# Performance work log

Hardware: AMD Instinct MI355X
Metric: run time of the kernel (lower is better)

Reference implementation:

```python
import jax, jax.numpy as jnp
import numpy as np

N_NODES = 100000
N_EDGES = 1600000
IN_FEATS = 256
DIMS = [IN_FEATS, 128, 64, 16, 40]


def setup_inputs() -> dict:
    key = jax.random.key(0)
    ks = jax.random.split(key, 3 + 2 * 4)
    x = jax.random.normal(ks[0], (N_NODES, IN_FEATS), dtype=jnp.float32)
    src = jax.random.randint(ks[1], (N_EDGES,), 0, N_NODES)
    dst = jax.random.randint(ks[2], (N_EDGES,), 0, N_NODES)
    inp = {"x": x, "src": src, "dst": dst}
    for i in range(4):
        fan_in = DIMS[i]
        inp[f"W{i+1}"] = jax.random.normal(ks[3 + 2 * i], (DIMS[i], DIMS[i + 1]), dtype=jnp.float32) / np.sqrt(fan_in)
        inp[f"b{i+1}"] = jnp.zeros((DIMS[i + 1],), dtype=jnp.float32)
    return inp


def reference(x, src, dst, W1, b1, W2, b2, W3, b3, W4, b4):
    n = x.shape[0]
    ones = jnp.ones(src.shape[0], dtype=x.dtype)
    # symmetric GCN normalization (DGL norm='both'); clamp deg>=1 like DGL
    deg_out = jnp.maximum(jax.ops.segment_sum(ones, src, num_segments=n), 1.0)
    deg_in = jnp.maximum(jax.ops.segment_sum(ones, dst, num_segments=n), 1.0)
    norm_src = jax.lax.rsqrt(deg_out)[:, None]  # [N,1]
    norm_dst = jax.lax.rsqrt(deg_in)[:, None]   # [N,1]

    def gconv(h, W, b, act):
        # project first (in_feats >= out_feats for every layer, matching DGL ordering)
        h = (h * norm_src) @ W                                   # [N, d_out]
        h = jax.ops.segment_sum(h[src], dst, num_segments=n)      # SpMM aggregate
        h = h * norm_dst + b
        return jax.nn.relu(h) if act else h

    h = gconv(x, W1, b1, True)
    h = gconv(h, W2, b2, True)
    h = gconv(h, W3, b3, True)
    h = gconv(h, W4, b4, False)
    return h
```

## Files before the change

kernel.cpp:

```cpp
#include <hip/hip_runtime.h>


typedef unsigned short ushort_t;
#define CAP 64

__device__ __forceinline__ void gload_lds16(const float4* g, float4* l) {
    __builtin_amdgcn_global_load_lds(
        (const __attribute__((address_space(1))) void*)g,
        (__attribute__((address_space(3))) void*)l, 16, 0, 0);
}

__device__ __forceinline__ ushort_t f2bf(float f) {
    unsigned u = __float_as_uint(f);
    u += 0x7FFFu + ((u >> 16) & 1u);
    return (ushort_t)(u >> 16);
}
__device__ __forceinline__ unsigned pack2bf(float a, float b) {
    return (unsigned)f2bf(a) | ((unsigned)f2bf(b) << 16);
}
__device__ __forceinline__ float nrm_of(int d) {
    return rsqrtf((float)(d > 1 ? d : 1));
}
#define BFLO(u) __uint_as_float((u) << 16)
#define BFHI(u) __uint_as_float((u) & 0xffff0000u)

template<int DIN, int DOUT, int RB, int KT, typename EPI>
__device__ __forceinline__ void proj_body(
        const float* __restrict__ in, const float* __restrict__ W,
        int N, int n0, float4* __restrict__ wlds, float4* __restrict__ xlds,
        EPI&& epi) {
    constexpr int CG  = DOUT / 4;
    constexpr int RPP = 256 / CG;
    constexpr int R4  = RB / RPP;
    constexpr int K4T = KT / 4;
    constexpr int NKT = DIN / KT;
    constexpr int XTILE = RB * K4T;
    constexpr int WTILE = KT * CG;

    const int tid  = threadIdx.x;
    const int wave = tid >> 6;
    const int lane = tid & 63;
    const int rp   = tid / CG;
    const int cg   = tid - rp * CG;

    float4 acc[R4];
#pragma unroll
    for (int r = 0; r < R4; ++r) acc[r] = make_float4(0.f, 0.f, 0.f, 0.f);

    for (int kt = 0; kt < NKT; ++kt) {
        const float4* wsrc = (const float4*)(W + (size_t)kt * KT * DOUT);
#pragma unroll
        for (int j = 0; j < WTILE / 256; ++j) {
            int base = j * 256 + wave * 64;
            gload_lds16(wsrc + base + lane, &wlds[base]);
        }
#pragma unroll
        for (int j = 0; j < XTILE / 256; ++j) {
            int base = j * 256 + wave * 64;
            int fi   = base + lane;
            int row  = fi / K4T;
            int k4   = fi - row * K4T;
            int k4s  = k4 ^ (row & (K4T - 1));
            int grow = n0 + row; if (grow >= N) grow = N - 1;
            const float4* gsrc = (const float4*)(in + (size_t)grow * DIN) + kt * K4T + k4s;
            gload_lds16(gsrc, &xlds[base]);
        }
        __syncthreads();
#pragma unroll 2
        for (int k4 = 0; k4 < K4T; ++k4) {
            float4 w0 = wlds[(k4 * 4 + 0) * CG + cg];
            float4 w1 = wlds[(k4 * 4 + 1) * CG + cg];
            float4 w2 = wlds[(k4 * 4 + 2) * CG + cg];
            float4 w3 = wlds[(k4 * 4 + 3) * CG + cg];
#pragma unroll
            for (int r = 0; r < R4; ++r) {
                int row = rp + r * RPP;
                float4 xv = xlds[row * K4T + (k4 ^ (row & (K4T - 1)))];
                acc[r].x = fmaf(xv.x, w0.x, acc[r].x);
                acc[r].y = fmaf(xv.x, w0.y, acc[r].y);
                acc[r].z = fmaf(xv.x, w0.z, acc[r].z);
                acc[r].w = fmaf(xv.x, w0.w, acc[r].w);
                acc[r].x = fmaf(xv.y, w1.x, acc[r].x);
                acc[r].y = fmaf(xv.y, w1.y, acc[r].y);
                acc[r].z = fmaf(xv.y, w1.z, acc[r].z);
                acc[r].w = fmaf(xv.y, w1.w, acc[r].w);
                acc[r].x = fmaf(xv.z, w2.x, acc[r].x);
                acc[r].y = fmaf(xv.z, w2.y, acc[r].y);
                acc[r].z = fmaf(xv.z, w2.z, acc[r].z);
                acc[r].w = fmaf(xv.z, w2.w, acc[r].w);
                acc[r].x = fmaf(xv.w, w3.x, acc[r].x);
                acc[r].y = fmaf(xv.w, w3.y, acc[r].y);
                acc[r].z = fmaf(xv.w, w3.z, acc[r].z);
                acc[r].w = fmaf(xv.w, w3.w, acc[r].w);
            }
        }
        __syncthreads();
    }
    epi(acc, rp, cg);
}

__device__ __forceinline__ void gather_l1_body(
        int n, int cb, const int* __restrict__ colp, const int* __restrict__ degO,
        const int* __restrict__ degI, const ushort_t* __restrict__ projbf,
        const float* __restrict__ bias, ushort_t* __restrict__ outbf) {
    constexpr int DOUT = 128;
    const int* cl = colp + (size_t)n * CAP;
    int dgi = degI[n];
    int dg = dgi > CAP ? CAP : dgi;
    float acc[8];
#pragma unroll
    for (int k = 0; k < 8; ++k) acc[k] = 0.f;
    int i = 0;
    for (; i + 4 <= dg; i += 4) {
        int4 ss = *(const int4*)(cl + i);
        uint4 v0 = *(const uint4*)(projbf + (size_t)ss.x * DOUT + cb * 8);
        uint4 v1 = *(const uint4*)(projbf + (size_t)ss.y * DOUT + cb * 8);
        uint4 v2 = *(const uint4*)(projbf + (size_t)ss.z * DOUT + cb * 8);
        uint4 v3 = *(const uint4*)(projbf + (size_t)ss.w * DOUT + cb * 8);
        float n0 = nrm_of(degO[ss.x]), n1 = nrm_of(degO[ss.y]);
        float n2 = nrm_of(degO[ss.z]), n3 = nrm_of(degO[ss.w]);
        acc[0] = fmaf(n0, BFLO(v0.x), fmaf(n1, BFLO(v1.x), fmaf(n2, BFLO(v2.x), fmaf(n3, BFLO(v3.x), acc[0]))));
        acc[1] = fmaf(n0, BFHI(v0.x), fmaf(n1, BFHI(v1.x), fmaf(n2, BFHI(v2.x), fmaf(n3, BFHI(v3.x), acc[1]))));
        acc[2] = fmaf(n0, BFLO(v0.y), fmaf(n1, BFLO(v1.y), fmaf(n2, BFLO(v2.y), fmaf(n3, BFLO(v3.y), acc[2]))));
        acc[3] = fmaf(n0, BFHI(v0.y), fmaf(n1, BFHI(v1.y), fmaf(n2, BFHI(v2.y), fmaf(n3, BFHI(v3.y), acc[3]))));
        acc[4] = fmaf(n0, BFLO(v0.z), fmaf(n1, BFLO(v1.z), fmaf(n2, BFLO(v2.z), fmaf(n3, BFLO(v3.z), acc[4]))));
        acc[5] = fmaf(n0, BFHI(v0.z), fmaf(n1, BFHI(v1.z), fmaf(n2, BFHI(v2.z), fmaf(n3, BFHI(v3.z), acc[5]))));
        acc[6] = fmaf(n0, BFLO(v0.w), fmaf(n1, BFLO(v1.w), fmaf(n2, BFLO(v2.w), fmaf(n3, BFLO(v3.w), acc[6]))));
        acc[7] = fmaf(n0, BFHI(v0.w), fmaf(n1, BFHI(v1.w), fmaf(n2, BFHI(v2.w), fmaf(n3, BFHI(v3.w), acc[7]))));
    }
    for (; i < dg; ++i) {
        int s0 = cl[i];
        uint4 v0 = *(const uint4*)(projbf + (size_t)s0 * DOUT + cb * 8);
        float ns0 = nrm_of(degO[s0]);
        acc[0] = fmaf(ns0, BFLO(v0.x), acc[0]);
        acc[1] = fmaf(ns0, BFHI(v0.x), acc[1]);
        acc[2] = fmaf(ns0, BFLO(v0.y), acc[2]);
        acc[3] = fmaf(ns0, BFHI(v0.y), acc[3]);
        acc[4] = fmaf(ns0, BFLO(v0.z), acc[4]);
        acc[5] = fmaf(ns0, BFHI(v0.z), acc[5]);
        acc[6] = fmaf(ns0, BFLO(v0.w), acc[6]);
        acc[7] = fmaf(ns0, BFHI(v0.w), acc[7]);
    }
    float nm = nrm_of(dgi);
    const float* bp = bias + cb * 8;
    float o[8];
#pragma unroll
    for (int k = 0; k < 8; ++k) o[k] = fmaxf(fmaf(acc[k], nm, bp[k]), 0.f);
    uint4 s;
    s.x = pack2bf(o[0], o[1]); s.y = pack2bf(o[2], o[3]);
    s.z = pack2bf(o[4], o[5]); s.w = pack2bf(o[6], o[7]);
    *(uint4*)(outbf + (size_t)n * DOUT + cb * 8) = s;
}

template<int DIN, int DOUT, int RB, int KT>
__global__ void __launch_bounds__(256) k_combA(
        const float* __restrict__ x, const float* __restrict__ W,
        ushort_t* __restrict__ outbf, int N,
        const int* __restrict__ src, const int* __restrict__ dst,
        int* __restrict__ degO, int* __restrict__ degI,
        int* __restrict__ colp, int E, int PB, int HTH, int NSPLIT) {
    constexpr int CG  = DOUT / 4;
    constexpr int RPP = 256 / CG;
    constexpr int R4  = RB / RPP;
    constexpr int K4T = KT / 4;
    __shared__ float4 wlds[KT * CG];
    __shared__ float4 xlds[RB * K4T];

    int bid = blockIdx.x, g = bid / 5, r = bid - g * 5;
    if (r == 4) {
        int i = g * 256 + (int)threadIdx.x;
        for (; i < E; i += HTH) {
            int s = src[i];
            int d = dst[i];
            atomicAdd(&degO[s], 1);
            if (d < NSPLIT) {
                int rk = atomicAdd(&degI[d], 1);
                if (rk < CAP) colp[(size_t)d * CAP + rk] = s;
            }
        }
        return;
    }
    int pidx = g * 4 + r;
    if (pidx >= PB) return;
    int n0 = pidx * RB;
    proj_body<DIN, DOUT, RB, KT>(x, W, N, n0, wlds, xlds,
        [&](float4 (&acc)[R4], int rp, int cg) {
#pragma unroll
            for (int rr = 0; rr < R4; ++rr) {
                int n = n0 + rp + rr * RPP;
                if (n < N) {
                    ushort4 s;
                    s.x = f2bf(acc[rr].x); s.y = f2bf(acc[rr].y);
                    s.z = f2bf(acc[rr].z); s.w = f2bf(acc[rr].w);
                    *(ushort4*)(outbf + (size_t)n * DOUT + cg * 4) = s;
                }
            }
        });
}

__global__ void __launch_bounds__(256) k_combB(
        const int* __restrict__ src, const int* __restrict__ dst,
        int* __restrict__ degI, int* __restrict__ colp,
        const int* __restrict__ degO, const ushort_t* __restrict__ projbf,
        const float* __restrict__ b1, ushort_t* __restrict__ h1bf,
        int NSPLIT, int E, int HTH) {
    int bid = blockIdx.x, g = bid / 5, r = bid - g * 5;
    if (r == 4) {
        int i = g * 256 + (int)threadIdx.x;
        for (; i < E; i += HTH) {
            int d = dst[i];
            if (d >= NSPLIT) {
                int rk = atomicAdd(&degI[d], 1);
                if (rk < CAP) colp[(size_t)d * CAP + rk] = src[i];
            }
        }
        return;
    }
    long t = ((long)(g * 4 + r)) * 256 + threadIdx.x;
    if (t >= (long)NSPLIT * 16) return;
    int n  = (int)(t >> 4);
    int cb = (int)(t & 15);
    gather_l1_body(n, cb, colp, degO, degI, projbf, b1, h1bf);
}

__global__ void __launch_bounds__(256) k_gather_l1(
        const int* __restrict__ colp, const int* __restrict__ degO,
        const int* __restrict__ degI, const ushort_t* __restrict__ projbf,
        const float* __restrict__ bias, ushort_t* __restrict__ outbf,
        int NSPLIT, int N) {
    long t = blockIdx.x * 256L + threadIdx.x;
    if (t >= (long)(N - NSPLIT) * 16) return;
    int n  = NSPLIT + (int)(t >> 4);
    int cb = (int)(t & 15);
    gather_l1_body(n, cb, colp, degO, degI, projbf, bias, outbf);
}

__global__ void __launch_bounds__(256) k_proj_l2bf(
        const ushort_t* __restrict__ in, const int* __restrict__ degO,
        const float* __restrict__ W, ushort_t* __restrict__ outbf, int N) {
    __shared__ float4 wlds[32 * 16];
    __shared__ uint4  xlds[64 * 4];
    const int tid = threadIdx.x;
    const int rp = tid >> 4, cg = tid & 15;
    int n0 = blockIdx.x * 64;

    float4 acc[4];
#pragma unroll
    for (int r = 0; r < 4; ++r) acc[r] = make_float4(0.f, 0.f, 0.f, 0.f);

    for (int kt = 0; kt < 4; ++kt) {
        const float4* wsrc = (const float4*)(W + (size_t)kt * 32 * 64);
        gload_lds16(wsrc + tid, &wlds[tid]);
        gload_lds16(wsrc + 256 + tid, &wlds[256 + tid]);
        {
            int row = tid >> 2, c = tid & 3;
            int cs = c ^ (row & 3);
            int grow = n0 + row; if (grow >= N) grow = N - 1;
            const uint4* gsrc = (const uint4*)(in + (size_t)grow * 128) + kt * 4 + cs;
            gload_lds16((const float4*)gsrc, (float4*)&xlds[tid]);
        }
        __syncthreads();
#pragma unroll
        for (int k8 = 0; k8 < 4; ++k8) {
            float4 w[8];
#pragma unroll
            for (int j = 0; j < 8; ++j) w[j] = wlds[(k8 * 8 + j) * 16 + cg];
#pragma unroll
            for (int r = 0; r < 4; ++r) {
                int row = rp + r * 16;
                uint4 xv = xlds[row * 4 + (k8 ^ (row & 3))];
                float xf[8] = { BFLO(xv.x), BFHI(xv.x), BFLO(xv.y), BFHI(xv.y),
                                BFLO(xv.z), BFHI(xv.z), BFLO(xv.w), BFHI(xv.w) };
#pragma unroll
                for (int j = 0; j < 8; ++j) {
                    acc[r].x = fmaf(xf[j], w[j].x, acc[r].x);
                    acc[r].y = fmaf(xf[j], w[j].y, acc[r].y);
                    acc[r].z = fmaf(xf[j], w[j].z, acc[r].z);
                    acc[r].w = fmaf(xf[j], w[j].w, acc[r].w);
                }
            }
        }
        __syncthreads();
    }
#pragma unroll
    for (int r = 0; r < 4; ++r) {
        int n = n0 + rp + r * 16;
        if (n < N) {
            float nm = nrm_of(degO[n]);
            ushort4 s;
            s.x = f2bf(acc[r].x * nm); s.y = f2bf(acc[r].y * nm);
            s.z = f2bf(acc[r].z * nm); s.w = f2bf(acc[r].w * nm);
            *(ushort4*)(outbf + (size_t)n * 64 + cg * 4) = s;
        }
    }
}

__global__ void __launch_bounds__(256) k_gather_fuse2(
        const int* __restrict__ colp, const int* __restrict__ degO,
        const int* __restrict__ degI, const ushort_t* __restrict__ p2bf,
        const float* __restrict__ b2, const float* __restrict__ W3,
        float* __restrict__ P3, int N) {
    constexpr int DOUT = 64;
    __shared__ float w3s[64 * 16];
    ((float4*)w3s)[threadIdx.x] = ((const float4*)W3)[threadIdx.x];
    __syncthreads();

    long t = blockIdx.x * 256L + threadIdx.x;
    int n = (int)(t >> 3);
    bool valid = n < N;
    if (!valid) n = N - 1;
    int cb = (int)(t & 7);
    int lane = threadIdx.x & 63;
    int gb = lane & ~7;

    const int* cl = colp + (size_t)n * CAP;
    int dgi = degI[n];
    int dg = dgi > CAP ? CAP : dgi;
    float acc[8];
#pragma unroll
    for (int k = 0; k < 8; ++k) acc[k] = 0.f;
    int i = 0;
    for (; i + 4 <= dg; i += 4) {
        int4 ss = *(const int4*)(cl + i);
        uint4 v0 = *(const uint4*)(p2bf + (size_t)ss.x * DOUT + cb * 8);
        uint4 v1 = *(const uint4*)(p2bf + (size_t)ss.y * DOUT + cb * 8);
        uint4 v2 = *(const uint4*)(p2bf + (size_t)ss.z * DOUT + cb * 8);
        uint4 v3 = *(const uint4*)(p2bf + (size_t)ss.w * DOUT + cb * 8);
        acc[0] += BFLO(v0.x) + BFLO(v1.x) + BFLO(v2.x) + BFLO(v3.x);
        acc[1] += BFHI(v0.x) + BFHI(v1.x) + BFHI(v2.x) + BFHI(v3.x);
        acc[2] += BFLO(v0.y) + BFLO(v1.y) + BFLO(v2.y) + BFLO(v3.y);
        acc[3] += BFHI(v0.y) + BFHI(v1.y) + BFHI(v2.y) + BFHI(v3.y);
        acc[4] += BFLO(v0.z) + BFLO(v1.z) + BFLO(v2.z) + BFLO(v3.z);
        acc[5] += BFHI(v0.z) + BFHI(v1.z) + BFHI(v2.z) + BFHI(v3.z);
        acc[6] += BFLO(v0.w) + BFLO(v1.w) + BFLO(v2.w) + BFLO(v3.w);
        acc[7] += BFHI(v0.w) + BFHI(v1.w) + BFHI(v2.w) + BFHI(v3.w);
    }
    for (; i < dg; ++i) {
        int s0 = cl[i];
        uint4 v0 = *(const uint4*)(p2bf + (size_t)s0 * DOUT + cb * 8);
        acc[0] += BFLO(v0.x); acc[1] += BFHI(v0.x);
        acc[2] += BFLO(v0.y); acc[3] += BFHI(v0.y);
        acc[4] += BFLO(v0.z); acc[5] += BFHI(v0.z);
        acc[6] += BFLO(v0.w); acc[7] += BFHI(v0.w);
    }
    float nm = nrm_of(dgi);
    float ns = nrm_of(degO[n]);
    const float* bp = b2 + cb * 8;
    float o[8];
#pragma unroll
    for (int k = 0; k < 8; ++k)
        o[k] = fmaxf(fmaf(acc[k], nm, bp[k]), 0.f) * ns;
    float y0 = 0.f, y1 = 0.f;
#pragma unroll
    for (int k = 0; k < 64; ++k) {
        float v = __shfl(o[k & 7], gb + (k >> 3), 64);
        y0 = fmaf(v, w3s[k * 16 + 2 * cb], y0);
        y1 = fmaf(v, w3s[k * 16 + 2 * cb + 1], y1);
    }
    if (valid) *(float2*)(P3 + (size_t)n * 16 + 2 * cb) = make_float2(y0, y1);
}

__global__ void __launch_bounds__(256) k_gather_l3(
        const int* __restrict__ colp, const int* __restrict__ degO,
        const int* __restrict__ degI, const float* __restrict__ proj,
        const float* __restrict__ bias, float* __restrict__ out, int N) {
    long t = blockIdx.x * 256L + threadIdx.x;
    if (t >= (long)N * 4) return;
    int n  = (int)(t >> 2);
    int cg = (int)(t & 3);
    const int* cl = colp + (size_t)n * CAP;
    int dgi = degI[n];
    int dg = dgi > CAP ? CAP : dgi;
    float4 a0 = make_float4(0.f, 0.f, 0.f, 0.f);
    float4 a1 = make_float4(0.f, 0.f, 0.f, 0.f);
    float4 a2 = make_float4(0.f, 0.f, 0.f, 0.f);
    float4 a3 = make_float4(0.f, 0.f, 0.f, 0.f);
    int i = 0;
    for (; i + 4 <= dg; i += 4) {
        int4 ss = *(const int4*)(cl + i);
        float4 v0 = *(const float4*)(proj + (size_t)ss.x * 16 + cg * 4);
        float4 v1 = *(const float4*)(proj + (size_t)ss.y * 16 + cg * 4);
        float4 v2 = *(const float4*)(proj + (size_t)ss.z * 16 + cg * 4);
        float4 v3 = *(const float4*)(proj + (size_t)ss.w * 16 + cg * 4);
        a0.x += v0.x; a0.y += v0.y; a0.z += v0.z; a0.w += v0.w;
        a1.x += v1.x; a1.y += v1.y; a1.z += v1.z; a1.w += v1.w;
        a2.x += v2.x; a2.y += v2.y; a2.z += v2.z; a2.w += v2.w;
        a3.x += v3.x; a3.y += v3.y; a3.z += v3.z; a3.w += v3.w;
    }
    for (; i < dg; ++i) {
        int s0 = cl[i];
        float4 v0 = *(const float4*)(proj + (size_t)s0 * 16 + cg * 4);
        a0.x += v0.x; a0.y += v0.y; a0.z += v0.z; a0.w += v0.w;
    }
    float4 s = make_float4(a0.x + a1.x + a2.x + a3.x, a0.y + a1.y + a2.y + a3.y,
                           a0.z + a1.z + a2.z + a3.z, a0.w + a1.w + a2.w + a3.w);
    float nm = nrm_of(dgi);
    float ns = nrm_of(degO[n]);
    float4 b = *(const float4*)(bias + cg * 4);
    float4 o;
    o.x = fmaxf(fmaf(s.x, nm, b.x), 0.f) * ns;
    o.y = fmaxf(fmaf(s.y, nm, b.y), 0.f) * ns;
    o.z = fmaxf(fmaf(s.z, nm, b.z), 0.f) * ns;
    o.w = fmaxf(fmaf(s.w, nm, b.w), 0.f) * ns;
    *(float4*)(out + (size_t)n * 16 + cg * 4) = o;
}

__global__ void __launch_bounds__(256) k_gather_fuse4(
        const int* __restrict__ colp, const int* __restrict__ degI,
        const float* __restrict__ t4, const float* __restrict__ W4,
        const float* __restrict__ b4, float* __restrict__ out, int N) {
    __shared__ float w4s[16 * 40];
    __shared__ float b4s[40];
    for (int i = threadIdx.x; i < 160; i += 256)
        ((float4*)w4s)[i] = ((const float4*)W4)[i];
    if (threadIdx.x < 40) b4s[threadIdx.x] = b4[threadIdx.x];
    __syncthreads();

    long t = blockIdx.x * 256L + threadIdx.x;
    int n = (int)(t >> 2);
    bool valid = n < N;
    if (!valid) n = N - 1;
    int cg = (int)(t & 3);
    int lane = threadIdx.x & 63;
    int gb = lane & ~3;

    const int* cl = colp + (size_t)n * CAP;
    int dgi = degI[n];
    int dg = dgi > CAP ? CAP : dgi;
    float4 a0 = make_float4(0.f, 0.f, 0.f, 0.f);
    float4 a1 = make_float4(0.f, 0.f, 0.f, 0.f);
    int i = 0;
    for (; i + 2 <= dg; i += 2) {
        int2 ss = *(const int2*)(cl + i);
        float4 v0 = *(const float4*)(t4 + (size_t)ss.x * 16 + cg * 4);
        float4 v1 = *(const float4*)(t4 + (size_t)ss.y * 16 + cg * 4);
        a0.x += v0.x; a0.y += v0.y; a0.z += v0.z; a0.w += v0.w;
        a1.x += v1.x; a1.y += v1.y; a1.z += v1.z; a1.w += v1.w;
    }
    if (i < dg) {
        int s0 = cl[i];
        float4 v0 = *(const float4*)(t4 + (size_t)s0 * 16 + cg * 4);
        a0.x += v0.x; a0.y += v0.y; a0.z += v0.z; a0.w += v0.w;
    }
    float av[4] = { a0.x + a1.x, a0.y + a1.y, a0.z + a1.z, a0.w + a1.w };

    float y[10];
#pragma unroll
    for (int jj = 0; jj < 10; ++jj) y[jj] = 0.f;
#pragma unroll
    for (int k = 0; k < 16; ++k) {
        float v = __shfl(av[k & 3], gb + (k >> 2), 64);
        const float* wr = w4s + k * 40 + cg * 10;
#pragma unroll
        for (int jj = 0; jj < 10; ++jj) y[jj] = fmaf(v, wr[jj], y[jj]);
    }
    if (valid) {
        float nm = nrm_of(dgi);
        float* dp = out + (size_t)n * 40 + cg * 10;
        const float* bp = b4s + cg * 10;
#pragma unroll
        for (int jj = 0; jj < 10; ++jj) dp[jj] = fmaf(y[jj], nm, bp[jj]);
    }
}

static inline int cdiv(long a, int b) { return (int)((a + b - 1) / b); }

extern "C" void kernel_launch(void* const* d_in, const int* in_sizes, int n_in,
                              void* d_out, int out_size, void* d_ws, size_t ws_size,
                              hipStream_t stream) {
    const float* x   = (const float*)d_in[0];
    const int*   src = (const int*)d_in[1];
    const int*   dst = (const int*)d_in[2];
    const float* W1 = (const float*)d_in[3];  const float* b1 = (const float*)d_in[4];
    const float* W2 = (const float*)d_in[5];  const float* b2 = (const float*)d_in[6];
    const float* W3 = (const float*)d_in[7];  const float* b3 = (const float*)d_in[8];
    const float* W4 = (const float*)d_in[9];  const float* b4 = (const float*)d_in[10];

    const int N = in_sizes[0] / 256;
    const int E = in_sizes[1];
    const int NSPLIT = ((N / 2) + 63) / 64 * 64;

    int* ws_i = (int*)d_ws;
    int* degO   = ws_i;
    int* degI   = ws_i + N;
    int* colp   = ws_i + 2 * (size_t)N;
    float* projb = (float*)(ws_i + 2 * (size_t)N + (size_t)N * CAP);
    float* hbuf  = projb + (size_t)N * 64;
    ushort_t* projbf = (ushort_t*)projb;
    ushort_t* h1bf   = (ushort_t*)hbuf;
    float* P3 = projb + (size_t)N * 32;

    int PB  = cdiv(N, 64);
    int G5A = cdiv(PB, 4);
    int HTHA = G5A * 256;

    long tA = (long)NSPLIT * 16;
    int GBB = cdiv(tA, 256);
    int G5B = cdiv(GBB, 4);
    int HTHB = G5B * 256;

    hipMemsetAsync(degO, 0, 2 * (size_t)N * sizeof(int), stream);
    k_combA<256, 128, 64, 32><<<5 * G5A, 256, 0, stream>>>(
        x, W1, projbf, N, src, dst, degO, degI, colp, E, PB, HTHA, NSPLIT);

    k_combB<<<5 * G5B, 256, 0, stream>>>(
        src, dst, degI, colp, degO, projbf, b1, h1bf, NSPLIT, E, HTHB);

    k_gather_l1<<<cdiv((long)(N - NSPLIT) * 16, 256), 256, 0, stream>>>(
        colp, degO, degI, projbf, b1, h1bf, NSPLIT, N);

    k_proj_l2bf<<<cdiv(N, 64), 256, 0, stream>>>(h1bf, degO, W2, projbf, N);
    k_gather_fuse2<<<cdiv((long)N * 8, 256), 256, 0, stream>>>(
        colp, degO, degI, projbf, b2, W3, P3, N);

    k_gather_l3<<<cdiv((long)N * 4, 256), 256, 0, stream>>>(
        colp, degO, degI, P3, b3, hbuf, N);

    k_gather_fuse4<<<cdiv((long)N * 4, 256), 256, 0, stream>>>(
        colp, degI, hbuf, W4, b4, (float*)d_out, N);
}
```

Baseline: 343.4 us.

## Split CSR build and layer-1 gather into three node ranges for deeper overlap

```diff
diff --git a/kernel.cpp b/kernel.cpp
--- a/kernel.cpp
+++ b/kernel.cpp
@@ -158,7 +158,7 @@
         ushort_t* __restrict__ outbf, int N,
         const int* __restrict__ src, const int* __restrict__ dst,
         int* __restrict__ degO, int* __restrict__ degI,
-        int* __restrict__ colp, int E, int PB, int HTH, int NSPLIT) {
+        int* __restrict__ colp, int E, int PB, int HTH, int S1) {
     constexpr int CG  = DOUT / 4;
     constexpr int RPP = 256 / CG;
     constexpr int R4  = RB / RPP;
@@ -173,7 +173,7 @@
             int s = src[i];
             int d = dst[i];
             atomicAdd(&degO[s], 1);
-            if (d < NSPLIT) {
+            if (d < S1) {
                 int rk = atomicAdd(&degI[d], 1);
                 if (rk < CAP) colp[(size_t)d * CAP + rk] = s;
             }
@@ -198,18 +198,18 @@
         });
 }
 
-__global__ void __launch_bounds__(256) k_combB(
+__global__ void __launch_bounds__(256) k_combP(
         const int* __restrict__ src, const int* __restrict__ dst,
         int* __restrict__ degI, int* __restrict__ colp,
         const int* __restrict__ degO, const ushort_t* __restrict__ projbf,
         const float* __restrict__ b1, ushort_t* __restrict__ h1bf,
-        int NSPLIT, int E, int HTH) {
+        int dlo, int dhi, int nlo, int nhi, int E, int HTH) {
     int bid = blockIdx.x, g = bid / 5, r = bid - g * 5;
     if (r == 4) {
         int i = g * 256 + (int)threadIdx.x;
         for (; i < E; i += HTH) {
             int d = dst[i];
-            if (d >= NSPLIT) {
+            if (d >= dlo && d < dhi) {
                 int rk = atomicAdd(&degI[d], 1);
                 if (rk < CAP) colp[(size_t)d * CAP + rk] = src[i];
             }
@@ -217,8 +217,8 @@
         return;
     }
     long t = ((long)(g * 4 + r)) * 256 + threadIdx.x;
-    if (t >= (long)NSPLIT * 16) return;
-    int n  = (int)(t >> 4);
+    if (t >= (long)(nhi - nlo) * 16) return;
+    int n  = nlo + (int)(t >> 4);
     int cb = (int)(t & 15);
     gather_l1_body(n, cb, colp, degO, degI, projbf, b1, h1bf);
 }
@@ -227,10 +227,10 @@
         const int* __restrict__ colp, const int* __restrict__ degO,
         const int* __restrict__ degI, const ushort_t* __restrict__ projbf,
         const float* __restrict__ bias, ushort_t* __restrict__ outbf,
-        int NSPLIT, int N) {
+        int nlo, int N) {
     long t = blockIdx.x * 256L + threadIdx.x;
-    if (t >= (long)(N - NSPLIT) * 16) return;
-    int n  = NSPLIT + (int)(t >> 4);
+    if (t >= (long)(N - nlo) * 16) return;
+    int n  = nlo + (int)(t >> 4);
     int cb = (int)(t & 15);
     gather_l1_body(n, cb, colp, degO, degI, projbf, bias, outbf);
 }
@@ -478,7 +478,8 @@
 
     const int N = in_sizes[0] / 256;
     const int E = in_sizes[1];
-    const int NSPLIT = ((N / 2) + 63) / 64 * 64;
+    const int S1 = (N / 3 + 63) / 64 * 64;
+    const int S2 = (2 * N / 3 + 63) / 64 * 64;
 
     int* ws_i = (int*)d_ws;
     int* degO   = ws_i;
@@ -494,20 +495,23 @@
     int G5A = cdiv(PB, 4);
     int HTHA = G5A * 256;
 
-    long tA = (long)NSPLIT * 16;
-    int GBB = cdiv(tA, 256);
-    int G5B = cdiv(GBB, 4);
+    int G5B = cdiv(cdiv((long)S1 * 16, 256), 4);
     int HTHB = G5B * 256;
+    int G5C = cdiv(cdiv((long)(S2 - S1) * 16, 256), 4);
+    int HTHC = G5C * 256;
 
     hipMemsetAsync(degO, 0, 2 * (size_t)N * sizeof(int), stream);
     k_combA<256, 128, 64, 32><<<5 * G5A, 256, 0, stream>>>(
-        x, W1, projbf, N, src, dst, degO, degI, colp, E, PB, HTHA, NSPLIT);
-
-    k_combB<<<5 * G5B, 256, 0, stream>>>(
-        src, dst, degI, colp, degO, projbf, b1, h1bf, NSPLIT, E, HTHB);
-
-    k_gather_l1<<<cdiv((long)(N - NSPLIT) * 16, 256), 256, 0, stream>>>(
-        colp, degO, degI, projbf, b1, h1bf, NSPLIT, N);
+        x, W1, projbf, N, src, dst, degO, degI, colp, E, PB, HTHA, S1);
+
+    k_combP<<<5 * G5B, 256, 0, stream>>>(
+        src, dst, degI, colp, degO, projbf, b1, h1bf, S1, S2, 0, S1, E, HTHB);
+
+    k_combP<<<5 * G5C, 256, 0, stream>>>(
+        src, dst, degI, colp, degO, projbf, b1, h1bf, S2, N, S1, S2, E, HTHC);
+
+    k_gather_l1<<<cdiv((long)(N - S2) * 16, 256), 256, 0, stream>>>(
+        colp, degO, degI, projbf, b1, h1bf, S2, N);
 
     k_proj_l2bf<<<cdiv(N, 64), 256, 0, stream>>>(h1bf, degO, W2, projbf, N);
     k_gather_fuse2<<<cdiv((long)N * 8, 256), 256, 0, stream>>>(
```

After: 352.3 us. 1.03x slower.
